# Optimization experiments

Measured on AMD Instinct MI355X. Metric: run time of the kernel, lower is better.

The kernel has to match this reference:

```python
import jax, jax.numpy as jnp
import numpy as np

COST_CLASS, COST_MASK, COST_DICE = 2.0, 5.0, 5.0
NUM_POINTS = 12544

def setup_inputs() -> dict:
    key = jax.random.key(0)
    k1, k2, k3, k4, k5 = jax.random.split(key, 5)
    bs, Q, K = 4, 100, 134
    H = W = 256
    M = 80
    P = H * W
    pred_logits = jax.random.normal(k1, (bs, Q, K), dtype=jnp.float32)
    pred_masks = jax.random.normal(k2, (bs, Q, H, W), dtype=jnp.float32)
    tgt_labels = jax.random.randint(k3, (M,), 0, K - 1, dtype=jnp.int32)
    # binary target masks, stored as float (matches .float() in torch code)
    tgt_masks = (jax.random.uniform(k4, (M, H, W)) > 0.5).astype(jnp.float32)
    # random subset of points without replacement (torch.randperm[:num_points])
    point_idx = jax.random.permutation(k5, P)[:NUM_POINTS].astype(jnp.int32)
    return {"pred_logits": pred_logits, "pred_masks": pred_masks,
            "tgt_labels": tgt_labels, "tgt_masks": tgt_masks,
            "point_idx": point_idx}

def reference(pred_logits, pred_masks, tgt_labels, tgt_masks, point_idx):
    bs, Q, K = pred_logits.shape
    N = bs * Q
    M = tgt_masks.shape[0]
    Pn = point_idx.shape[0]

    # class cost: -p[n, tgt_id[m]]
    out_prob = jax.nn.softmax(pred_logits.reshape(N, K), axis=-1)
    tgt_ids = jnp.clip(tgt_labels.astype(jnp.int32), 0, K - 1)
    cost_class = -out_prob[:, tgt_ids]                      # (N, M)

    # sampled mask logits / targets
    x = pred_masks.reshape(N, -1)[:, point_idx]             # (N, Pn) logits
    y = tgt_masks.reshape(M, -1)[:, point_idx]              # (M, Pn) binary float

    # BCE-with-logits cost, separable form:
    # mean_p[softplus(x) - x*y] = mean_p softplus(x) - (x @ y^T)/Pn
    sp_mean = jnp.mean(jax.nn.softplus(x), axis=-1)         # (N,)
    xy = jnp.einsum('np,mp->nm', x, y)                      # (N, M)
    cost_mask = sp_mean[:, None] - xy / Pn

    # dice cost
    s = jax.nn.sigmoid(x)                                   # (N, Pn)
    numer = 2.0 * jnp.einsum('np,mp->nm', s, y)             # (N, M)
    denom = jnp.sum(s, axis=-1)[:, None] + jnp.sum(y, axis=-1)[None, :]
    cost_dice = 1.0 - (numer + 1.0) / (denom + 1.0)

    C = COST_CLASS * cost_class + COST_MASK * cost_mask + COST_DICE * cost_dice
    return C.reshape(bs, Q, M)
```

## Files before the change

kernel.cpp:

```cpp
#include <hip/hip_runtime.h>
#include <math.h>

#define N_ROWS 400
#define M_ROWS 80
#define MPAD   96
#define K_CLS  134
#define PN     12544
#define PFULL  65536
#define NSUB   25
#define TSTEPS 2048
#define KSPLIT 64
#define TPB    (TSTEPS / KSPLIT)

typedef __attribute__((ext_vector_type(4))) float  f32x4;
typedef __attribute__((ext_vector_type(8))) __bf16 bf16x8;

__device__ __forceinline__ float wave_reduce_sum(float v) {
#pragma unroll
    for (int off = 32; off > 0; off >>= 1) v += __shfl_down(v, off, 64);
    return v;
}

__global__ void softmax_stats_kernel(const float* __restrict__ logits,
                                     float* __restrict__ rowmax,
                                     float* __restrict__ rowsum) {
    int n = blockIdx.x;
    const float* row = logits + n * K_CLS;
    int l = threadIdx.x;
    float mx = -1e30f;
    for (int k = l; k < K_CLS; k += 64) mx = fmaxf(mx, row[k]);
#pragma unroll
    for (int off = 32; off > 0; off >>= 1) mx = fmaxf(mx, __shfl_down(mx, off, 64));
    mx = __shfl(mx, 0, 64);
    float se = 0.f;
    for (int k = l; k < K_CLS; k += 64) se += expf(row[k] - mx);
    se = wave_reduce_sum(se);
    if (l == 0) { rowmax[n] = mx; rowsum[n] = se; }
}

__global__ void scatter_wgt_kernel(const int* __restrict__ point_idx,
                                   float* __restrict__ wgt) {
    int i = blockIdx.x * blockDim.x + threadIdx.x;
    if (i < PN) wgt[point_idx[i]] = 1.0f;
}

__global__ __launch_bounds__(256) void yformat_kernel(
        const float* __restrict__ tgt_masks, const float* __restrict__ wgt,
        __bf16* __restrict__ Yb, float* __restrict__ ysum) {
    int j = blockIdx.x >> 4;
    int tchunk = blockIdx.x & 15;
    int tloc = threadIdx.x >> 6;
    int lane = threadIdx.x & 63;
    int colL = lane & 15, quad = lane >> 4;
    int m = 16 * j + colL;
    const float* yrow = tgt_masks + (size_t)m * PFULL;
    bf16x8* out = (bf16x8*)Yb;
    float part = 0.f;
    for (int t = tchunk * 128 + tloc; t < tchunk * 128 + 128; t += 4) {
        int k = t * 32 + quad * 8;
        f32x4 w0 = *(const f32x4*)(wgt + k);
        f32x4 w1 = *(const f32x4*)(wgt + k + 4);
        bf16x8 v;
        if (m < M_ROWS) {
            f32x4 y0 = *(const f32x4*)(yrow + k);
            f32x4 y1 = *(const f32x4*)(yrow + k + 4);
#pragma unroll
            for (int jj = 0; jj < 4; ++jj) {
                float v0 = w0[jj] * y0[jj], v1 = w1[jj] * y1[jj];
                part += v0 + v1;
                v[jj] = (__bf16)v0; v[jj + 4] = (__bf16)v1;
            }
        } else if (m == M_ROWS) {
#pragma unroll
            for (int jj = 0; jj < 4; ++jj) { v[jj] = (__bf16)w0[jj]; v[jj + 4] = (__bf16)w1[jj]; }
        } else {
#pragma unroll
            for (int jj = 0; jj < 8; ++jj) v[jj] = (__bf16)0.f;
        }
        out[(size_t)(t * 6 + j) * 64 + lane] = v;
    }
    if (m < M_ROWS) atomicAdd(&ysum[m], part);
}

__global__ __launch_bounds__(256) void mfma_kernel(
        const float* __restrict__ pred_masks,
        const __bf16* __restrict__ Yb,
        float* __restrict__ xyacc, float* __restrict__ syacc,
        float* __restrict__ ssum, float* __restrict__ spsum) {
    int wave = threadIdx.x >> 6;
    int lane = threadIdx.x & 63;
    int nsub = blockIdx.x * 4 + wave;
    int nclamp = nsub < NSUB ? nsub : NSUB - 1;
    int n0 = nclamp * 16;
    int colL = lane & 15;
    int quad = lane >> 4;
    int tbase = blockIdx.y * TPB;

    const float* arow = pred_masks + (size_t)(n0 + colL) * PFULL;
    const bf16x8* Yfrag = (const bf16x8*)Yb;

    f32x4 accX[5], accS[6], accSP;
    f32x4 zero = {0.f, 0.f, 0.f, 0.f};
#pragma unroll
    for (int j = 0; j < 5; ++j) accX[j] = zero;
#pragma unroll
    for (int j = 0; j < 6; ++j) accS[j] = zero;
    accSP = zero;

    auto load = [&](int i, f32x4& A0, f32x4& A1, bf16x8* B) {
        int t = tbase + i;
        const f32x4* p = (const f32x4*)(arow + (size_t)t * 32 + quad * 8);
        A0 = p[0]; A1 = p[1];
        const bf16x8* q = Yfrag + (size_t)(t * 6) * 64 + lane;
#pragma unroll
        for (int j = 0; j < 6; ++j) B[j] = q[(size_t)j * 64];
    };

    auto compute = [&](f32x4 A0, f32x4 A1, const bf16x8* B) {
        bf16x8 aX, aS, aSP;
#pragma unroll
        for (int jj = 0; jj < 8; ++jj) {
            float x  = (jj < 4) ? A0[jj & 3] : A1[jj & 3];
            float ax = fabsf(x);
            float e  = __expf(-ax);
            float inv = __builtin_amdgcn_rcpf(1.0f + e);
            float sig = (x >= 0.f) ? inv : e * inv;
            float sp  = fmaxf(x, 0.f) + __logf(1.0f + e);
            aX[jj] = (__bf16)x; aS[jj] = (__bf16)sig; aSP[jj] = (__bf16)sp;
        }
#pragma unroll
        for (int j = 0; j < 5; ++j)
            accX[j] = __builtin_amdgcn_mfma_f32_16x16x32_bf16(aX, B[j], accX[j], 0, 0, 0);
#pragma unroll
        for (int j = 0; j < 6; ++j)
            accS[j] = __builtin_amdgcn_mfma_f32_16x16x32_bf16(aS, B[j], accS[j], 0, 0, 0);
        accSP = __builtin_amdgcn_mfma_f32_16x16x32_bf16(aSP, B[5], accSP, 0, 0, 0);
    };

    f32x4 A0a, A1a, A0b, A1b;
    bf16x8 Ba[6], Bb[6];
    load(0, A0a, A1a, Ba);
    for (int i = 0; i < TPB; i += 2) {
        load(i + 1, A0b, A1b, Bb);
        compute(A0a, A1a, Ba);
        if (i + 2 < TPB) load(i + 2, A0a, A1a, Ba);
        compute(A0b, A1b, Bb);
    }

    if (nsub < NSUB) {
#pragma unroll
        for (int j = 0; j < 5; ++j)
#pragma unroll
            for (int r = 0; r < 4; ++r) {
                int n = n0 + quad * 4 + r;
                int m = 16 * j + colL;
                atomicAdd(&xyacc[n * M_ROWS + m], accX[j][r]);
                atomicAdd(&syacc[n * M_ROWS + m], accS[j][r]);
            }
        if (colL == 0) {
#pragma unroll
            for (int r = 0; r < 4; ++r) {
                int n = n0 + quad * 4 + r;
                atomicAdd(&ssum[n], accS[5][r]);
                atomicAdd(&spsum[n], accSP[r]);
            }
        }
    }
}

__global__ void combine_kernel(const float* __restrict__ logits,
                               const int* __restrict__ tgt_labels,
                               const float* __restrict__ rowmax,
                               const float* __restrict__ rowsum,
                               const float* __restrict__ spsum,
                               const float* __restrict__ ssum,
                               const float* __restrict__ ysum,
                               const float* __restrict__ xyacc,
                               const float* __restrict__ syacc,
                               float* __restrict__ out) {
    int idx = blockIdx.x * blockDim.x + threadIdx.x;
    if (idx >= N_ROWS * M_ROWS) return;
    int n = idx / M_ROWS, m = idx % M_ROWS;
    int tid = tgt_labels[m];
    tid = min(max(tid, 0), K_CLS - 1);
    float p = expf(logits[n * K_CLS + tid] - rowmax[n]) / rowsum[n];
    float cost_class = -p;
    float cost_mask = (spsum[n] - xyacc[idx]) * (1.0f / PN);
    float cost_dice = 1.f - (2.f * syacc[idx] + 1.f) / (ssum[n] + ysum[m] + 1.f);
    out[idx] = 2.f * cost_class + 5.f * cost_mask + 5.f * cost_dice;
}

extern "C" void kernel_launch(void* const* d_in, const int* in_sizes, int n_in,
                              void* d_out, int out_size, void* d_ws, size_t ws_size,
                              hipStream_t stream) {
    const float* pred_logits = (const float*)d_in[0];
    const float* pred_masks  = (const float*)d_in[1];
    const int*   tgt_labels  = (const int*)d_in[2];
    const float* tgt_masks   = (const float*)d_in[3];
    const int*   point_idx   = (const int*)d_in[4];
    float* out = (float*)d_out;

    char* ws = (char*)d_ws;
    size_t off = 0;
    auto carve = [&](size_t nfloats) {
        float* p = (float*)(ws + off);
        off += ((nfloats * 4 + 255) / 256) * 256;
        return p;
    };
    float* xyacc  = carve((size_t)N_ROWS * M_ROWS);
    float* syacc  = carve((size_t)N_ROWS * M_ROWS);
    float* spsum  = carve(N_ROWS);
    float* ssum   = carve(N_ROWS);
    float* ysum   = carve(M_ROWS);
    float* wgt    = carve(PFULL);
    size_t zero_bytes = off;
    float* rowmax = carve(N_ROWS);
    float* rowsum = carve(N_ROWS);
    __bf16* Yb = (__bf16*)(ws + off);
    off += (size_t)TSTEPS * 6 * 1024;
    (void)ws_size;

    hipMemsetAsync(xyacc, 0, zero_bytes, stream);
    scatter_wgt_kernel<<<(PN + 255) / 256, 256, 0, stream>>>(point_idx, wgt);
    softmax_stats_kernel<<<N_ROWS, 64, 0, stream>>>(pred_logits, rowmax, rowsum);
    yformat_kernel<<<96, 256, 0, stream>>>(tgt_masks, wgt, Yb, ysum);
    dim3 grid((NSUB + 3) / 4, KSPLIT);
    mfma_kernel<<<grid, 256, 0, stream>>>(pred_masks, Yb, xyacc, syacc, ssum, spsum);
    combine_kernel<<<(N_ROWS * M_ROWS + 255) / 256, 256, 0, stream>>>(
        pred_logits, tgt_labels, rowmax, rowsum, spsum, ssum, ysum, xyacc, syacc, out);
}
```

Baseline: 247.3 us.

## Gather sampled points before GEMM instead of dense masked GEMM over all pixels

Replaces the dense weighted GEMM over all 65536 pixels with explicit gathers of the sampled points. X gets its sigmoid and softplus computed per sample and is stored as bf16, and Y is gathered into MFMA fragment layout. The GEMM then runs only over 12544 points with row sums precomputed, which avoids transcendental and MFMA work on unsampled pixels. In exchange it adds an intermediate bf16 buffer round trip and uses random-index gathers.

```diff
diff --git a/kernel.cpp b/kernel.cpp
--- a/kernel.cpp
+++ b/kernel.cpp
@@ -3,14 +3,13 @@
 
 #define N_ROWS 400
 #define M_ROWS 80
-#define MPAD   96
 #define K_CLS  134
 #define PN     12544
 #define PFULL  65536
 #define NSUB   25
-#define TSTEPS 2048
-#define KSPLIT 64
-#define TPB    (TSTEPS / KSPLIT)
+#define TSTEPS 392
+#define KSPLIT 56
+#define TPB    7
 
 typedef __attribute__((ext_vector_type(4))) float  f32x4;
 typedef __attribute__((ext_vector_type(8))) __bf16 bf16x8;
@@ -38,113 +37,114 @@
     if (l == 0) { rowmax[n] = mx; rowsum[n] = se; }
 }
 
-__global__ void scatter_wgt_kernel(const int* __restrict__ point_idx,
-                                   float* __restrict__ wgt) {
-    int i = blockIdx.x * blockDim.x + threadIdx.x;
-    if (i < PN) wgt[point_idx[i]] = 1.0f;
-}
-
-__global__ __launch_bounds__(256) void yformat_kernel(
-        const float* __restrict__ tgt_masks, const float* __restrict__ wgt,
+__global__ __launch_bounds__(512) void gather_x_kernel(
+        const float* __restrict__ pred_masks, const int* __restrict__ point_idx,
+        __bf16* __restrict__ Xb, __bf16* __restrict__ Sb,
+        float* __restrict__ spsum, float* __restrict__ ssum) {
+    int n = blockIdx.x;
+    const float* row = pred_masks + (size_t)n * PFULL;
+    __bf16* xrow = Xb + (size_t)n * PN;
+    __bf16* srow = Sb + (size_t)n * PN;
+    float ssp = 0.f, sss = 0.f;
+#pragma unroll 4
+    for (int p = threadIdx.x; p < PN; p += 512) {
+        int idx = point_idx[p];
+        float x  = row[idx];
+        float ax = fabsf(x);
+        float e  = __expf(-ax);
+        float inv = __builtin_amdgcn_rcpf(1.0f + e);
+        float sig = (x >= 0.f) ? inv : e * inv;
+        float sp  = fmaxf(x, 0.f) + __logf(1.0f + e);
+        xrow[p] = (__bf16)x;
+        srow[p] = (__bf16)sig;
+        ssp += sp; sss += sig;
+    }
+    __shared__ float sm1[8], sm2[8];
+    float w1 = wave_reduce_sum(ssp), w2 = wave_reduce_sum(sss);
+    int lane = threadIdx.x & 63, wid = threadIdx.x >> 6;
+    if (lane == 0) { sm1[wid] = w1; sm2[wid] = w2; }
+    __syncthreads();
+    if (threadIdx.x == 0) {
+        float a = 0.f, b = 0.f;
+#pragma unroll
+        for (int i = 0; i < 8; ++i) { a += sm1[i]; b += sm2[i]; }
+        spsum[n] = a; ssum[n] = b;
+    }
+}
+
+__global__ __launch_bounds__(256) void gather_y_kernel(
+        const float* __restrict__ tgt_masks, const int* __restrict__ point_idx,
         __bf16* __restrict__ Yb, float* __restrict__ ysum) {
-    int j = blockIdx.x >> 4;
-    int tchunk = blockIdx.x & 15;
-    int tloc = threadIdx.x >> 6;
-    int lane = threadIdx.x & 63;
+    int j = blockIdx.x / 49;
+    int tchunk = blockIdx.x % 49;
+    int wave = threadIdx.x >> 6, lane = threadIdx.x & 63;
     int colL = lane & 15, quad = lane >> 4;
     int m = 16 * j + colL;
     const float* yrow = tgt_masks + (size_t)m * PFULL;
     bf16x8* out = (bf16x8*)Yb;
-    float part = 0.f;
-    for (int t = tchunk * 128 + tloc; t < tchunk * 128 + 128; t += 4) {
-        int k = t * 32 + quad * 8;
-        f32x4 w0 = *(const f32x4*)(wgt + k);
-        f32x4 w1 = *(const f32x4*)(wgt + k + 4);
+    float acc = 0.f;
+#pragma unroll
+    for (int u = 0; u < 2; ++u) {
+        int t = tchunk * 8 + wave * 2 + u;
+        int k0 = t * 32 + quad * 8;
+        int idx[8];
+        *(int4*)(idx)     = *(const int4*)(point_idx + k0);
+        *(int4*)(idx + 4) = *(const int4*)(point_idx + k0 + 4);
         bf16x8 v;
-        if (m < M_ROWS) {
-            f32x4 y0 = *(const f32x4*)(yrow + k);
-            f32x4 y1 = *(const f32x4*)(yrow + k + 4);
-#pragma unroll
-            for (int jj = 0; jj < 4; ++jj) {
-                float v0 = w0[jj] * y0[jj], v1 = w1[jj] * y1[jj];
-                part += v0 + v1;
-                v[jj] = (__bf16)v0; v[jj + 4] = (__bf16)v1;
-            }
-        } else if (m == M_ROWS) {
-#pragma unroll
-            for (int jj = 0; jj < 4; ++jj) { v[jj] = (__bf16)w0[jj]; v[jj + 4] = (__bf16)w1[jj]; }
-        } else {
-#pragma unroll
-            for (int jj = 0; jj < 8; ++jj) v[jj] = (__bf16)0.f;
+#pragma unroll
+        for (int jj = 0; jj < 8; ++jj) {
+            float y = yrow[idx[jj]];
+            v[jj] = (__bf16)y;
+            acc += y;
         }
-        out[(size_t)(t * 6 + j) * 64 + lane] = v;
-    }
-    if (m < M_ROWS) atomicAdd(&ysum[m], part);
-}
-
-__global__ __launch_bounds__(256) void mfma_kernel(
-        const float* __restrict__ pred_masks,
+        out[(size_t)(t * 5 + j) * 64 + lane] = v;
+    }
+    acc += __shfl_down(acc, 32, 64);
+    acc += __shfl_down(acc, 16, 64);
+    if (quad == 0) atomicAdd(&ysum[m], acc);
+}
+
+__global__ __launch_bounds__(256) void mfma_gemm_kernel(
+        const __bf16* __restrict__ Xb, const __bf16* __restrict__ Sb,
         const __bf16* __restrict__ Yb,
-        float* __restrict__ xyacc, float* __restrict__ syacc,
-        float* __restrict__ ssum, float* __restrict__ spsum) {
-    int wave = threadIdx.x >> 6;
-    int lane = threadIdx.x & 63;
+        float* __restrict__ xyacc, float* __restrict__ syacc) {
+    int wave = threadIdx.x >> 6, lane = threadIdx.x & 63;
     int nsub = blockIdx.x * 4 + wave;
     int nclamp = nsub < NSUB ? nsub : NSUB - 1;
     int n0 = nclamp * 16;
-    int colL = lane & 15;
-    int quad = lane >> 4;
+    int colL = lane & 15, quad = lane >> 4;
     int tbase = blockIdx.y * TPB;
 
-    const float* arow = pred_masks + (size_t)(n0 + colL) * PFULL;
+    const __bf16* xrow = Xb + (size_t)(n0 + colL) * PN;
+    const __bf16* srow = Sb + (size_t)(n0 + colL) * PN;
     const bf16x8* Yfrag = (const bf16x8*)Yb;
 
-    f32x4 accX[5], accS[6], accSP;
+    f32x4 accX[5], accS[5];
     f32x4 zero = {0.f, 0.f, 0.f, 0.f};
 #pragma unroll
-    for (int j = 0; j < 5; ++j) accX[j] = zero;
-#pragma unroll
-    for (int j = 0; j < 6; ++j) accS[j] = zero;
-    accSP = zero;
-
-    auto load = [&](int i, f32x4& A0, f32x4& A1, bf16x8* B) {
+    for (int j = 0; j < 5; ++j) { accX[j] = zero; accS[j] = zero; }
+
+    bf16x8 Abuf[2], Sbuf[2], Bbuf[2][5];
+    auto load = [&](int i, int b) {
         int t = tbase + i;
-        const f32x4* p = (const f32x4*)(arow + (size_t)t * 32 + quad * 8);
-        A0 = p[0]; A1 = p[1];
-        const bf16x8* q = Yfrag + (size_t)(t * 6) * 64 + lane;
-#pragma unroll
-        for (int j = 0; j < 6; ++j) B[j] = q[(size_t)j * 64];
+        size_t ko = (size_t)t * 32 + quad * 8;
+        Abuf[b] = *(const bf16x8*)(xrow + ko);
+        Sbuf[b] = *(const bf16x8*)(srow + ko);
+        const bf16x8* q = Yfrag + (size_t)(t * 5) * 64 + lane;
+#pragma unroll
+        for (int j = 0; j < 5; ++j) Bbuf[b][j] = q[(size_t)j * 64];
     };
 
-    auto compute = [&](f32x4 A0, f32x4 A1, const bf16x8* B) {
-        bf16x8 aX, aS, aSP;
-#pragma unroll
-        for (int jj = 0; jj < 8; ++jj) {
-            float x  = (jj < 4) ? A0[jj & 3] : A1[jj & 3];
-            float ax = fabsf(x);
-            float e  = __expf(-ax);
-            float inv = __builtin_amdgcn_rcpf(1.0f + e);
-            float sig = (x >= 0.f) ? inv : e * inv;
-            float sp  = fmaxf(x, 0.f) + __logf(1.0f + e);
-            aX[jj] = (__bf16)x; aS[jj] = (__bf16)sig; aSP[jj] = (__bf16)sp;
+    load(0, 0);
+#pragma unroll
+    for (int i = 0; i < TPB; ++i) {
+        int b = i & 1;
+        if (i + 1 < TPB) load(i + 1, b ^ 1);
+#pragma unroll
+        for (int j = 0; j < 5; ++j) {
+            accX[j] = __builtin_amdgcn_mfma_f32_16x16x32_bf16(Abuf[b], Bbuf[b][j], accX[j], 0, 0, 0);
+            accS[j] = __builtin_amdgcn_mfma_f32_16x16x32_bf16(Sbuf[b], Bbuf[b][j], accS[j], 0, 0, 0);
         }
-#pragma unroll
-        for (int j = 0; j < 5; ++j)
-            accX[j] = __builtin_amdgcn_mfma_f32_16x16x32_bf16(aX, B[j], accX[j], 0, 0, 0);
-#pragma unroll
-        for (int j = 0; j < 6; ++j)
-            accS[j] = __builtin_amdgcn_mfma_f32_16x16x32_bf16(aS, B[j], accS[j], 0, 0, 0);
-        accSP = __builtin_amdgcn_mfma_f32_16x16x32_bf16(aSP, B[5], accSP, 0, 0, 0);
-    };
-
-    f32x4 A0a, A1a, A0b, A1b;
-    bf16x8 Ba[6], Bb[6];
-    load(0, A0a, A1a, Ba);
-    for (int i = 0; i < TPB; i += 2) {
-        load(i + 1, A0b, A1b, Bb);
-        compute(A0a, A1a, Ba);
-        if (i + 2 < TPB) load(i + 2, A0a, A1a, Ba);
-        compute(A0b, A1b, Bb);
     }
 
     if (nsub < NSUB) {
@@ -157,14 +157,6 @@
                 atomicAdd(&xyacc[n * M_ROWS + m], accX[j][r]);
                 atomicAdd(&syacc[n * M_ROWS + m], accS[j][r]);
             }
-        if (colL == 0) {
-#pragma unroll
-            for (int r = 0; r < 4; ++r) {
-                int n = n0 + quad * 4 + r;
-                atomicAdd(&ssum[n], accS[5][r]);
-                atomicAdd(&spsum[n], accSP[r]);
-            }
-        }
     }
 }
 
@@ -202,30 +194,30 @@
 
     char* ws = (char*)d_ws;
     size_t off = 0;
-    auto carve = [&](size_t nfloats) {
-        float* p = (float*)(ws + off);
-        off += ((nfloats * 4 + 255) / 256) * 256;
+    auto carve = [&](size_t nbytes) {
+        char* p = ws + off;
+        off += (nbytes + 255) & ~(size_t)255;
         return p;
     };
-    float* xyacc  = carve((size_t)N_ROWS * M_ROWS);
-    float* syacc  = carve((size_t)N_ROWS * M_ROWS);
-    float* spsum  = carve(N_ROWS);
-    float* ssum   = carve(N_ROWS);
-    float* ysum   = carve(M_ROWS);
-    float* wgt    = carve(PFULL);
+    float* xyacc = (float*)carve((size_t)N_ROWS * M_ROWS * 4);
+    float* syacc = (float*)carve((size_t)N_ROWS * M_ROWS * 4);
+    float* ysum  = (float*)carve(M_ROWS * 4);
     size_t zero_bytes = off;
-    float* rowmax = carve(N_ROWS);
-    float* rowsum = carve(N_ROWS);
-    __bf16* Yb = (__bf16*)(ws + off);
-    off += (size_t)TSTEPS * 6 * 1024;
+    float* spsum  = (float*)carve(N_ROWS * 4);
+    float* ssum   = (float*)carve(N_ROWS * 4);
+    float* rowmax = (float*)carve(N_ROWS * 4);
+    float* rowsum = (float*)carve(N_ROWS * 4);
+    __bf16* Xb = (__bf16*)carve((size_t)N_ROWS * PN * 2);
+    __bf16* Sb = (__bf16*)carve((size_t)N_ROWS * PN * 2);
+    __bf16* Yb = (__bf16*)carve((size_t)TSTEPS * 5 * 1024);
     (void)ws_size;
 
     hipMemsetAsync(xyacc, 0, zero_bytes, stream);
-    scatter_wgt_kernel<<<(PN + 255) / 256, 256, 0, stream>>>(point_idx, wgt);
+    gather_x_kernel<<<N_ROWS, 512, 0, stream>>>(pred_masks, point_idx, Xb, Sb, spsum, ssum);
+    gather_y_kernel<<<5 * 49, 256, 0, stream>>>(tgt_masks, point_idx, Yb, ysum);
     softmax_stats_kernel<<<N_ROWS, 64, 0, stream>>>(pred_logits, rowmax, rowsum);
-    yformat_kernel<<<96, 256, 0, stream>>>(tgt_masks, wgt, Yb, ysum);
     dim3 grid((NSUB + 3) / 4, KSPLIT);
-    mfma_kernel<<<grid, 256, 0, stream>>>(pred_masks, Yb, xyacc, syacc, ssum, spsum);
+    mfma_gemm_kernel<<<grid, 256, 0, stream>>>(Xb, Sb, Yb, xyacc, syacc);
     combine_kernel<<<(N_ROWS * M_ROWS + 255) / 256, 256, 0, stream>>>(
         pred_logits, tgt_labels, rowmax, rowsum, spsum, ssum, ysum, xyacc, syacc, out);
 }
```

Measured after the change: 252.2 us. No clear change (+2.0%).
